# Kernel tuning notes

Measured on AMD Instinct MI355X. Metric: run time of the kernel, lower is better.

## Reference

```python
import jax, jax.numpy as jnp
import numpy as np

B, IN_DIM, H1, H2, C = 8192, 1024, 2048, 2048, 1000
E, TOP_K, RH = 8, 2, 512
QB = 127.0
EPS = 1e-5


def _ste_round(x):
    # straight-through estimator round (BitNet-style)
    return x + jax.lax.stop_gradient(jnp.round(x) - x)


def _act_quant(x):
    # per-token absmax 8-bit activation quantization
    s = QB / jnp.clip(jnp.max(jnp.abs(x), axis=-1, keepdims=True), EPS, None)
    return jnp.clip(_ste_round(x * s), -QB, QB) / s


def _weight_quant(w):
    # ternary 1.58b weight quantization, per-tensor mean-abs scale
    s = jnp.clip(jnp.mean(jnp.abs(w)), EPS, None)
    return jnp.clip(_ste_round(w / s), -1.0, 1.0) * s


def _bit_linear(x, w, b):
    return _act_quant(x) @ _weight_quant(w).T + b


def setup_inputs() -> dict:
    key = jax.random.key(0)
    ks = jax.random.split(key, 12)
    def init(k, shape, fan_in):
        return (jax.random.normal(k, shape, dtype=jnp.float32) / np.sqrt(fan_in)).astype(jnp.float32)
    return {
        "x":  jax.random.normal(ks[0], (B, IN_DIM), dtype=jnp.float32),
        "Wr1": init(ks[1], (RH, IN_DIM), IN_DIM),
        "br1": jnp.zeros((RH,), jnp.float32),
        "Wr2": init(ks[2], (E, RH), RH),
        "br2": jnp.zeros((E,), jnp.float32),
        "W1": init(ks[3], (E, H1, IN_DIM), IN_DIM),
        "b1": jnp.zeros((E, H1), jnp.float32),
        "W2": init(ks[4], (E, H2, H1), H1),
        "b2": jnp.zeros((E, H2), jnp.float32),
        "W3": init(ks[5], (E, C, H2), H2),
        "b3": jnp.zeros((E, C), jnp.float32),
    }


def _forward(x, Wr1, br1, Wr2, br2, W1, b1, W2, b2, W3, b3):
    # Router (eval mode: dropout off)
    h = jax.nn.relu(x @ Wr1.T + br1)
    router_probs = jax.nn.softmax(h @ Wr2.T + br2, axis=1)       # [B, E]
    topk_vals, topk_idx = jax.lax.top_k(router_probs, TOP_K)     # [B, K]

    # dense gate matrix: gate[b,e] = sum_k topk_vals[b,k] * (topk_idx[b,k]==e)
    gates = jnp.sum(topk_vals[..., None] * jax.nn.one_hot(topk_idx, E, dtype=x.dtype), axis=1)  # [B, E]

    def expert(w1, c1, w2, c2, w3, c3):
        y = jax.nn.relu(_bit_linear(x, w1, c1))
        y = jax.nn.relu(_bit_linear(y, w2, c2))
        return _bit_linear(y, w3, c3)                             # [B, C]

    out_all = jax.vmap(expert)(W1, b1, W2, b2, W3, b3)            # [E, B, C]
    outputs = jnp.einsum('ebc,be->bc', out_all, gates) / TOP_K    # [B, C]
    load_balancing_loss = jnp.zeros((), x.dtype)                  # eval mode
    return outputs, router_probs, load_balancing_loss


def reference(x, Wr1, br1, Wr2, br2, W1, b1, W2, b2, W3, b3):
    return _forward(x, Wr1, br1, Wr2, br2, W1, b1, W2, b2, W3, b3)
```

## Files before the change

### kernel.cpp

```cpp
#include <hip/hip_runtime.h>
#include <stdint.h>

#define DEV static __device__ __forceinline__

typedef int v4i __attribute__((ext_vector_type(4)));
typedef short v8s __attribute__((ext_vector_type(8)));
typedef float v4f __attribute__((ext_vector_type(4)));

constexpr int B_T   = 8192;
constexpr int IN_D  = 1024;
constexpr int H1D   = 2048;
constexpr int H2D   = 2048;
constexpr int CDIM  = 1000;
constexpr int NEXP  = 8;
constexpr int RHD   = 512;
constexpr float QBF  = 127.0f;
constexpr float EPSF = 1e-5f;
constexpr int NSLOT = 2 * B_T;
constexpr int MAXT  = 72;
constexpr float GAP_DELTA = 2e-3f;

DEV void load_lds16(const void* g, void* l) {
  __builtin_amdgcn_global_load_lds(
      (const __attribute__((address_space(1))) uint32_t*)(uintptr_t)g,
      (__attribute__((address_space(3))) uint32_t*)(uint32_t)(uintptr_t)l,
      16, 0, 0);
}

DEV uint32_t pack4(float a, float b, float c, float d, float s) {
  int q0 = (int)rintf(a * s); q0 = q0 > 127 ? 127 : (q0 < -127 ? -127 : q0);
  int q1 = (int)rintf(b * s); q1 = q1 > 127 ? 127 : (q1 < -127 ? -127 : q1);
  int q2 = (int)rintf(c * s); q2 = q2 > 127 ? 127 : (q2 < -127 ? -127 : q2);
  int q3 = (int)rintf(d * s); q3 = q3 > 127 ? 127 : (q3 < -127 ? -127 : q3);
  return (uint32_t)(uint8_t)q0 | ((uint32_t)(uint8_t)q1 << 8) |
         ((uint32_t)(uint8_t)q2 << 16) | ((uint32_t)(uint8_t)q3 << 24);
}

DEV uint16_t f2bf(float f) {
  uint32_t u = __float_as_uint(f);
  return (uint16_t)((u + 0x7FFFu + ((u >> 16) & 1u)) >> 16);
}
DEV float bf2f(uint16_t h) { return __uint_as_float((uint32_t)h << 16); }

__global__ __launch_bounds__(256) void wabs_reduce(const float* __restrict__ W,
                                                   long perExpert, int tbase,
                                                   double* __restrict__ partial) {
  int e = blockIdx.y;
  const float4* base = (const float4*)(W + (long)e * perExpert);
  long n4 = perExpert >> 2;
  double s = 0.0;
  for (long i = (long)blockIdx.x * 256 + threadIdx.x; i < n4; i += 32L * 256L) {
    float4 v = base[i];
    s += (double)fabsf(v.x) + (double)fabsf(v.y) + (double)fabsf(v.z) + (double)fabsf(v.w);
  }
  __shared__ double red[256];
  red[threadIdx.x] = s;
  __syncthreads();
  for (int st = 128; st > 0; st >>= 1) {
    if ((int)threadIdx.x < st) red[threadIdx.x] += red[threadIdx.x + st];
    __syncthreads();
  }
  if (threadIdx.x == 0) partial[(long)(tbase + e) * 32 + blockIdx.x] = red[0];
}

__global__ void finalize_scales(const double* __restrict__ partial, float* __restrict__ swf) {
  int t = threadIdx.x;
  if (t >= 24) return;
  double s = 0.0;
  for (int i = 0; i < 32; ++i) s += partial[t * 32 + i];
  long cnt = (t < 8) ? (long)H1D * IN_D : (t < 16) ? (long)H2D * H1D : (long)CDIM * H2D;
  float mean = (float)(s / (double)cnt);
  swf[t] = fmaxf(mean, EPSF);
}

__global__ __launch_bounds__(256) void wquant(const float* __restrict__ W,
                                              int8_t* __restrict__ Wq,
                                              const float* __restrict__ swf, int tbase,
                                              long perExpert, long total4) {
  long i = (long)blockIdx.x * 256 + threadIdx.x;
  if (i >= total4) return;
  long e = (i * 4) / perExpert;
  float s = swf[tbase + (int)e];
  float4 v = ((const float4*)W)[i];
  float t0 = fminf(fmaxf(rintf(v.x / s), -1.f), 1.f);
  float t1 = fminf(fmaxf(rintf(v.y / s), -1.f), 1.f);
  float t2 = fminf(fmaxf(rintf(v.z / s), -1.f), 1.f);
  float t3 = fminf(fmaxf(rintf(v.w / s), -1.f), 1.f);
  uint32_t p = (uint32_t)(uint8_t)(int8_t)t0 | ((uint32_t)(uint8_t)(int8_t)t1 << 8) |
               ((uint32_t)(uint8_t)(int8_t)t2 << 16) | ((uint32_t)(uint8_t)(int8_t)t3 << 24);
  ((uint32_t*)Wq)[i] = p;
}

template <int WIDTH>
__global__ __launch_bounds__(256) void actquant(const float* __restrict__ X,
                                                int8_t* __restrict__ Xq,
                                                float* __restrict__ rcp_out) {
  constexpr int PT = WIDTH / 1024;
  const int row = blockIdx.x;
  const int tid = threadIdx.x;
  const float4* src = (const float4*)(X + (size_t)row * WIDTH);
  float4 v[PT];
  float mx = 0.f;
#pragma unroll
  for (int p = 0; p < PT; ++p) {
    v[p] = src[tid * PT + p];
    mx = fmaxf(mx, fmaxf(fmaxf(fabsf(v[p].x), fabsf(v[p].y)),
                         fmaxf(fabsf(v[p].z), fabsf(v[p].w))));
  }
#pragma unroll
  for (int m = 1; m < 64; m <<= 1) mx = fmaxf(mx, __shfl_xor(mx, m));
  __shared__ float wmax[4];
  const int lane = tid & 63, w = tid >> 6;
  if (lane == 0) wmax[w] = mx;
  __syncthreads();
  mx = fmaxf(fmaxf(wmax[0], wmax[1]), fmaxf(wmax[2], wmax[3]));
  const float M = fmaxf(mx, EPSF);
  const float s = QBF / M;
  uint32_t* dst = (uint32_t*)(Xq + (size_t)row * WIDTH);
#pragma unroll
  for (int p = 0; p < PT; ++p)
    dst[tid * PT + p] = pack4(v[p].x, v[p].y, v[p].z, v[p].w, s);
  if (tid == 0) rcp_out[row] = M / QBF;
}

__global__ __launch_bounds__(256) void split_bf16(const float* __restrict__ src,
                                                  uint16_t* __restrict__ hi,
                                                  uint16_t* __restrict__ lo, long n4) {
  long i = (long)blockIdx.x * 256 + threadIdx.x;
  if (i >= n4) return;
  float4 v = ((const float4*)src)[i];
  ushort4 h, l;
  float f[4] = {v.x, v.y, v.z, v.w};
  uint16_t hh[4], ll[4];
#pragma unroll
  for (int j = 0; j < 4; ++j) {
    hh[j] = f2bf(f[j]);
    ll[j] = f2bf(f[j] - bf2f(hh[j]));
  }
  h.x = hh[0]; h.y = hh[1]; h.z = hh[2]; h.w = hh[3];
  l.x = ll[0]; l.y = ll[1]; l.z = ll[2]; l.w = ll[3];
  ((ushort4*)hi)[i] = h;
  ((ushort4*)lo)[i] = l;
}

__global__ __launch_bounds__(256, 1) void router_mfma(
    const uint16_t* __restrict__ xh, const uint16_t* __restrict__ xl,
    const uint16_t* __restrict__ wh, const uint16_t* __restrict__ wl,
    const float* __restrict__ br1, float* __restrict__ h) {
  __shared__ __align__(16) int8_t smem[2][65536];
  const int tid = threadIdx.x;
  const int lane = tid & 63, wid = tid >> 6;
  const int wm = wid >> 1, wn = wid & 1;
  const int row0 = blockIdx.x * 128, col0 = blockIdx.y * 128;

  const uint16_t* mats[4] = {xh, xl, wh, wl};
  const int rb[4] = {row0, row0, col0, col0};
  const uint8_t* src[16];
#pragma unroll
  for (int R = 0; R < 4; ++R)
#pragma unroll
    for (int i = 0; i < 4; ++i) {
      int p = i * 256 + tid;
      int r = p >> 3, c = p & 7;
      int cs = c ^ (r & 7);
      src[R * 4 + i] = (const uint8_t*)mats[R] + ((long)(rb[R] + r) * IN_D + cs * 8) * 2;
    }

  v4f acc[4][4] = {};
  auto stage = [&](int buf, int kt) {
#pragma unroll
    for (int R = 0; R < 4; ++R)
#pragma unroll
      for (int i = 0; i < 4; ++i)
        load_lds16(src[R * 4 + i] + kt * 128,
                   &smem[buf][R * 16384 + i * 4096 + wid * 1024]);
  };

  stage(0, 0);
  asm volatile("s_waitcnt vmcnt(0)" ::: "memory");
  __syncthreads();
  int buf = 0;
  for (int kt = 0; kt < 16; ++kt) {
    if (kt + 1 < 16) stage(buf ^ 1, kt + 1);
#pragma unroll
    for (int ks = 0; ks < 2; ++ks) {
      v8s ah[4], al[4], bh[4], bl[4];
#pragma unroll
      for (int m = 0; m < 4; ++m) {
        int r = wm * 64 + m * 16 + (lane & 15);
        int ch = (ks * 4 + (lane >> 4)) ^ (r & 7);
        ah[m] = *(const v8s*)&smem[buf][r * 128 + ch * 16];
        al[m] = *(const v8s*)&smem[buf][16384 + r * 128 + ch * 16];
      }
#pragma unroll
      for (int n = 0; n < 4; ++n) {
        int r = wn * 64 + n * 16 + (lane & 15);
        int ch = (ks * 4 + (lane >> 4)) ^ (r & 7);
        bh[n] = *(const v8s*)&smem[buf][32768 + r * 128 + ch * 16];
        bl[n] = *(const v8s*)&smem[buf][49152 + r * 128 + ch * 16];
      }
#pragma unroll
      for (int m = 0; m < 4; ++m)
#pragma unroll
        for (int n = 0; n < 4; ++n) {
          acc[m][n] = __builtin_amdgcn_mfma_f32_16x16x32_bf16(ah[m], bh[n], acc[m][n], 0, 0, 0);
          acc[m][n] = __builtin_amdgcn_mfma_f32_16x16x32_bf16(ah[m], bl[n], acc[m][n], 0, 0, 0);
          acc[m][n] = __builtin_amdgcn_mfma_f32_16x16x32_bf16(al[m], bh[n], acc[m][n], 0, 0, 0);
        }
    }
    asm volatile("s_waitcnt vmcnt(0)" ::: "memory");
    __syncthreads();
    buf ^= 1;
  }

  const int rbase = (lane >> 4) * 4;
  const int cfr = lane & 15;
#pragma unroll
  for (int m = 0; m < 4; ++m)
#pragma unroll
    for (int rg = 0; rg < 4; ++rg) {
      int row = row0 + wm * 64 + m * 16 + rbase + rg;
#pragma unroll
      for (int n = 0; n < 4; ++n) {
        int col = col0 + wn * 64 + n * 16 + cfr;
        h[(long)row * RHD + col] = fmaxf(acc[m][n][rg] + br1[col], 0.f);
      }
    }
}

__global__ __launch_bounds__(256) void router_stage2(const float* __restrict__ h,
                                                     const float* __restrict__ Wr2,
                                                     const float* __restrict__ br2,
                                                     float* __restrict__ probs,
                                                     int* __restrict__ idxg,
                                                     float* __restrict__ gvg,
                                                     int* __restrict__ scount,
                                                     int* __restrict__ suspects) {
  __shared__ float w2s[NEXP * RHD];
  const int tid = threadIdx.x;
  for (int i = tid; i < NEXP * RHD; i += 256) w2s[i] = Wr2[i];
  __syncthreads();
  const int lane = tid & 63, w = tid >> 6;
  const int b = blockIdx.x * 4 + w;
  const float* hrow = h + (long)b * RHD;
  float4 v0 = *(const float4*)&hrow[lane * 8];
  float4 v1 = *(const float4*)&hrow[lane * 8 + 4];
  float hr[8] = {v0.x, v0.y, v0.z, v0.w, v1.x, v1.y, v1.z, v1.w};
  float lg[8];
#pragma unroll
  for (int e = 0; e < 8; ++e) {
    float p = 0.f;
#pragma unroll
    for (int j = 0; j < 8; ++j) p = fmaf(hr[j], w2s[e * RHD + lane * 8 + j], p);
#pragma unroll
    for (int m = 1; m < 64; m <<= 1) p += __shfl_xor(p, m);
    lg[e] = p + br2[e];
  }
  if (lane == 0) {
    float mx = lg[0];
#pragma unroll
    for (int e = 1; e < 8; ++e) mx = fmaxf(mx, lg[e]);
    float ex[8], sum = 0.f;
#pragma unroll
    for (int e = 0; e < 8; ++e) { ex[e] = expf(lg[e] - mx); sum += ex[e]; }
#pragma unroll
    for (int e = 0; e < 8; ++e) probs[(long)b * 8 + e] = ex[e] / sum;
    int i0 = 0; float b0 = lg[0];
#pragma unroll
    for (int e = 1; e < 8; ++e) if (lg[e] > b0) { b0 = lg[e]; i0 = e; }
    int i1 = -1; float b1v = -3.4e38f;
#pragma unroll
    for (int e = 0; e < 8; ++e) if (e != i0 && lg[e] > b1v) { b1v = lg[e]; i1 = e; }
    float b2v = -3.4e38f;
#pragma unroll
    for (int e = 0; e < 8; ++e) if (e != i0 && e != i1 && lg[e] > b2v) b2v = lg[e];
    idxg[b * 2 + 0] = i0; idxg[b * 2 + 1] = i1;
    gvg[b * 2 + 0] = ex[i0] / sum; gvg[b * 2 + 1] = ex[i1] / sum;
    if (b1v - b2v < GAP_DELTA) {
      int p = atomicAdd(scount, 1);
      if (p < B_T) suspects[p] = b;
    }
  }
}

__global__ __launch_bounds__(256) void router_fixup(const float* __restrict__ x,
                                                    const float* __restrict__ Wr1,
                                                    const float* __restrict__ br1,
                                                    const float* __restrict__ Wr2,
                                                    const float* __restrict__ br2,
                                                    const int* __restrict__ suspects,
                                                    const int* __restrict__ scount,
                                                    float* __restrict__ probs,
                                                    int* __restrict__ idxg,
                                                    float* __restrict__ gvg) {
  __shared__ float xr[IN_D];
  __shared__ float hr[RHD];
  __shared__ float lgs[NEXP];
  const int n = *scount;
  const int tid = threadIdx.x;
  for (int s = blockIdx.x; s < n && s < B_T; s += 128) {
    const int b = suspects[s];
    __syncthreads();
    for (int i = tid; i < IN_D; i += 256) xr[i] = x[(long)b * IN_D + i];
    __syncthreads();
    {
      const int c0 = tid * 2, c1 = tid * 2 + 1;
      const float* w0 = Wr1 + (long)c0 * IN_D;
      const float* w1 = Wr1 + (long)c1 * IN_D;
      float a0 = 0.f, a1 = 0.f;
      for (int k = 0; k < IN_D; ++k) {
        float xv = xr[k];
        a0 = fmaf(xv, w0[k], a0);
        a1 = fmaf(xv, w1[k], a1);
      }
      hr[c0] = fmaxf(a0 + br1[c0], 0.f);
      hr[c1] = fmaxf(a1 + br1[c1], 0.f);
    }
    __syncthreads();
    if (tid < NEXP) {
      const float* w2 = Wr2 + (long)tid * RHD;
      float a = 0.f;
      for (int k = 0; k < RHD; ++k) a = fmaf(hr[k], w2[k], a);
      lgs[tid] = a + br2[tid];
    }
    __syncthreads();
    if (tid == 0) {
      float lg[8];
#pragma unroll
      for (int e = 0; e < 8; ++e) lg[e] = lgs[e];
      float mx = lg[0];
#pragma unroll
      for (int e = 1; e < 8; ++e) mx = fmaxf(mx, lg[e]);
      float ex[8], sum = 0.f;
#pragma unroll
      for (int e = 0; e < 8; ++e) { ex[e] = expf(lg[e] - mx); sum += ex[e]; }
#pragma unroll
      for (int e = 0; e < 8; ++e) probs[(long)b * 8 + e] = ex[e] / sum;
      int i0 = 0; float b0 = lg[0];
#pragma unroll
      for (int e = 1; e < 8; ++e) if (lg[e] > b0) { b0 = lg[e]; i0 = e; }
      int i1 = -1; float b1v = -3.4e38f;
#pragma unroll
      for (int e = 0; e < 8; ++e) if (e != i0 && lg[e] > b1v) { b1v = lg[e]; i1 = e; }
      idxg[b * 2 + 0] = i0; idxg[b * 2 + 1] = i1;
      gvg[b * 2 + 0] = ex[i0] / sum; gvg[b * 2 + 1] = ex[i1] / sum;
    }
  }
}

__global__ __launch_bounds__(256) void hist_block(const int* __restrict__ idxg,
                                                  int* __restrict__ bc) {
  __shared__ int hloc[NEXP];
  const int t = threadIdx.x;
  if (t < NEXP) hloc[t] = 0;
  __syncthreads();
  int a = blockIdx.x * 256 + t;
  atomicAdd(&hloc[idxg[a]], 1);
  __syncthreads();
  if (t < NEXP) bc[blockIdx.x * NEXP + t] = hloc[t];
}

__global__ void scan_all(const int* __restrict__ bc, int* __restrict__ blockbase,
                         int* __restrict__ ntiles, int* __restrict__ te,
                         int* __restrict__ ts, int* __restrict__ tc,
                         float* __restrict__ loss_out) {
  __shared__ int counts[NEXP], basep[NEXP];
  const int t = threadIdx.x;
  if (t < NEXP) {
    int s = 0;
    for (int b = 0; b < 64; ++b) s += bc[b * NEXP + t];
    counts[t] = s;
  }
  __syncthreads();
  if (t == 0) {
    int acc = 0, nb = 0;
    for (int e = 0; e < NEXP; ++e) {
      basep[e] = acc;
      int c = counts[e];
      int nt = (c + 255) >> 8;
      for (int i = 0; i < nt; ++i) {
        te[nb] = e; ts[nb] = acc + i * 256; tc[nb] = min(256, c - i * 256); ++nb;
      }
      acc += c;
    }
    *ntiles = nb;
    *loss_out = 0.f;
  }
  __syncthreads();
  if (t < NEXP) {
    int run = basep[t];
    for (int b = 0; b < 64; ++b) { blockbase[b * NEXP + t] = run; run += bc[b * NEXP + t]; }
  }
}

__global__ __launch_bounds__(256) void place2(const int* __restrict__ idxg,
                                              const int* __restrict__ blockbase,
                                              int* __restrict__ token_list,
                                              int* __restrict__ slotmap) {
  __shared__ int cur[NEXP];
  const int t = threadIdx.x;
  if (t < NEXP) cur[t] = blockbase[blockIdx.x * NEXP + t];
  __syncthreads();
  int a = blockIdx.x * 256 + t;
  int e = idxg[a];
  int pos = atomicAdd(&cur[e], 1);
  token_list[pos] = a >> 1;
  slotmap[a] = pos;
}

template <int KDIM, bool INDIRECT, bool RELU, bool FINAL>
__global__ __launch_bounds__(512, 1) void gemm_i8(
    const int8_t* __restrict__ Aq, const int8_t* __restrict__ Wq,
    const float* __restrict__ swf_layer, const float* __restrict__ rcp_act,
    const float* __restrict__ bias, const int* __restrict__ te,
    const int* __restrict__ ts, const int* __restrict__ tc,
    const int* __restrict__ ntiles_p, const int* __restrict__ token_list,
    float* __restrict__ Yout, int Nvalid) {
  if ((int)blockIdx.x >= *ntiles_p) return;
  extern __shared__ __align__(16) int8_t smem_dyn[];
  const int t = blockIdx.x;
  const int e = te[t], row0 = ts[t], rcount = tc[t];
  const int col0 = blockIdx.y * 256;
  const int tid = threadIdx.x;
  const int lane = tid & 63, wid = tid >> 6;
  const int wm = wid >> 2, wn = wid & 3;

  const int8_t* srcA[4];
  const int8_t* srcB[4];
#pragma unroll
  for (int i = 0; i < 4; ++i) {
    int p = i * 512 + tid;
    int r = p >> 3, c = p & 7;
    int cs = c ^ ((r >> 1) & 7);
    int ar = row0 + min(r, rcount - 1);
    long arow = INDIRECT ? (long)token_list[ar] : (long)ar;
    srcA[i] = Aq + arow * KDIM + cs * 16;
    int br = min(col0 + r, Nvalid - 1);
    srcB[i] = Wq + ((long)e * Nvalid + br) * (long)KDIM + cs * 16;
  }

  auto stage = [&](int buf, int kt) {
#pragma unroll
    for (int i = 0; i < 4; ++i) {
      int off = buf * 65536 + (i * 512 + (wid << 6)) * 16;
      load_lds16(srcA[i] + kt * 128, &smem_dyn[off]);
      load_lds16(srcB[i] + kt * 128, &smem_dyn[32768 + off]);
    }
  };

  v4i acc[8][4] = {};
  constexpr int KT = KDIM / 128;
  stage(0, 0);
  asm volatile("s_waitcnt vmcnt(0)" ::: "memory");
  __builtin_amdgcn_s_barrier();
  int buf = 0;
  for (int kt = 0; kt < KT; ++kt) {
    if (kt + 1 < KT) {
      stage(buf ^ 1, kt + 1);
      asm volatile("s_waitcnt vmcnt(8)" ::: "memory");
    } else {
      asm volatile("s_waitcnt vmcnt(0)" ::: "memory");
    }
    __builtin_amdgcn_s_barrier();
    __builtin_amdgcn_sched_barrier(0);
    const int8_t* As = &smem_dyn[buf * 65536];
    const int8_t* Bs = &smem_dyn[buf * 65536 + 32768];
#pragma unroll
    for (int ks = 0; ks < 2; ++ks) {
      v4i bv[4];
#pragma unroll
      for (int n = 0; n < 4; ++n) {
        int r = wn * 64 + n * 16 + (lane & 15);
        int cs = (ks * 4 + (lane >> 4)) ^ ((r >> 1) & 7);
        bv[n] = *(const v4i*)&Bs[r * 128 + cs * 16];
      }
#pragma unroll
      for (int m = 0; m < 8; ++m) {
        int r = wm * 128 + m * 16 + (lane & 15);
        int cs = (ks * 4 + (lane >> 4)) ^ ((r >> 1) & 7);
        v4i av = *(const v4i*)&As[r * 128 + cs * 16];
#pragma unroll
        for (int n = 0; n < 4; ++n)
          acc[m][n] = __builtin_amdgcn_mfma_i32_16x16x64_i8(av, bv[n], acc[m][n], 0, 0, 0);
      }
    }
    __builtin_amdgcn_sched_barrier(0);
    __builtin_amdgcn_s_barrier();
    buf ^= 1;
  }

  const float sw = swf_layer[e];
  const int rbase = (lane >> 4) * 4;
  const int cfr = lane & 15;
  const float* bias_e = bias + (long)e * Nvalid;
#pragma unroll
  for (int m = 0; m < 8; ++m) {
#pragma unroll
    for (int rg = 0; rg < 4; ++rg) {
      int trow = wm * 128 + m * 16 + rbase + rg;
      if (trow >= rcount) continue;
      int slot = row0 + trow;
      float rcp = rcp_act[INDIRECT ? token_list[slot] : slot];
      float dq = sw * rcp;
      if (!FINAL) {
        float* yrow = Yout + (long)slot * 2048;
#pragma unroll
        for (int n = 0; n < 4; ++n) {
          int o = col0 + wn * 64 + n * 16 + cfr;
          float v = (float)acc[m][n][rg] * dq + bias_e[o];
          if (RELU) v = fmaxf(v, 0.f);
          yrow[o] = v;
        }
      } else {
        float* zrow = Yout + (long)slot * 1024;
#pragma unroll
        for (int n = 0; n < 4; ++n) {
          int o = col0 + wn * 64 + n * 16 + cfr;
          float bb = bias_e[min(o, Nvalid - 1)];
          zrow[o] = (float)acc[m][n][rg] * dq + bb;
        }
      }
    }
  }
}

__global__ __launch_bounds__(256) void combine(const float* __restrict__ z,
                                               const int* __restrict__ slotmap,
                                               const float* __restrict__ gvg,
                                               float* __restrict__ out) {
  const int b = blockIdx.x;
  const int c = threadIdx.x;
  if (c >= 250) return;
  const int s0 = slotmap[b * 2], s1 = slotmap[b * 2 + 1];
  const float g0 = gvg[b * 2] * 0.5f, g1 = gvg[b * 2 + 1] * 0.5f;
  float4 a = *(const float4*)(z + (long)s0 * 1024 + c * 4);
  float4 q = *(const float4*)(z + (long)s1 * 1024 + c * 4);
  float4 o = {g0 * a.x + g1 * q.x, g0 * a.y + g1 * q.y,
              g0 * a.z + g1 * q.z, g0 * a.w + g1 * q.w};
  *(float4*)(out + (long)b * CDIM + c * 4) = o;
}

extern "C" void kernel_launch(void* const* d_in, const int* in_sizes, int n_in,
                              void* d_out, int out_size, void* d_ws, size_t ws_size,
                              hipStream_t stream) {
  const float* x   = (const float*)d_in[0];
  const float* Wr1 = (const float*)d_in[1];
  const float* br1 = (const float*)d_in[2];
  const float* Wr2 = (const float*)d_in[3];
  const float* br2 = (const float*)d_in[4];
  const float* W1  = (const float*)d_in[5];
  const float* b1  = (const float*)d_in[6];
  const float* W2  = (const float*)d_in[7];
  const float* b2  = (const float*)d_in[8];
  const float* W3  = (const float*)d_in[9];
  const float* b3  = (const float*)d_in[10];
  float* out = (float*)d_out;
  char* ws = (char*)d_ws;

  size_t off = 0;
  auto alloc = [&](size_t sz) { size_t r = off; off = (off + sz + 255) & ~(size_t)255; return r; };
  size_t O_META  = alloc(8192);
  size_t O_SUSP  = alloc(B_T * sizeof(int));
  size_t O_PART  = alloc(24 * 32 * sizeof(double));
  size_t O_SWF   = alloc(24 * sizeof(float));
  size_t O_RCPX  = alloc(B_T * sizeof(float));
  size_t O_IDX   = alloc(B_T * 2 * sizeof(int));
  size_t O_GVG   = alloc(B_T * 2 * sizeof(float));
  size_t O_TLIST = alloc(NSLOT * sizeof(int));
  size_t O_SLOT  = alloc(B_T * 2 * sizeof(int));
  size_t O_S1    = alloc(NSLOT * sizeof(float));
  size_t O_S2    = alloc(NSLOT * sizeof(float));
  size_t O_XQ    = alloc((size_t)B_T * IN_D);
  size_t O_WQ1   = alloc((size_t)NEXP * H1D * IN_D);
  size_t O_WQ2   = alloc((size_t)NEXP * H2D * H1D);
  size_t O_WQ3   = alloc((size_t)NEXP * CDIM * H2D);
  size_t O_YQ    = alloc((size_t)NSLOT * 2048);
  size_t O_YBIG  = alloc((size_t)NSLOT * 2048 * sizeof(float));
  (void)ws_size; (void)in_sizes; (void)n_in;

  int*    te     = (int*)(ws + O_META);
  int*    tsv    = te + 144;
  int*    tcv    = tsv + 144;
  int*    ntiles = tcv + 144;
  int*    bc     = ntiles + 4;
  int*    bbase  = bc + 512;
  int*    scount = bbase + 512;
  int*    susp   = (int*)(ws + O_SUSP);
  double* part   = (double*)(ws + O_PART);
  float*  swf    = (float*)(ws + O_SWF);
  float*  rcpx   = (float*)(ws + O_RCPX);
  int*    idxg   = (int*)(ws + O_IDX);
  float*  gvg    = (float*)(ws + O_GVG);
  int*    tlist  = (int*)(ws + O_TLIST);
  int*    slotmap= (int*)(ws + O_SLOT);
  float*  s1     = (float*)(ws + O_S1);
  float*  s2     = (float*)(ws + O_S2);
  int8_t* Xq     = (int8_t*)(ws + O_XQ);
  int8_t* wq1    = (int8_t*)(ws + O_WQ1);
  int8_t* wq2    = (int8_t*)(ws + O_WQ2);
  int8_t* wq3    = (int8_t*)(ws + O_WQ3);
  int8_t* Yq     = (int8_t*)(ws + O_YQ);
  float*  Ybig   = (float*)(ws + O_YBIG);
  float*  h      = Ybig;
  float*  zbuf   = Ybig;

  char* ybytes = (char*)Ybig;
  uint16_t* xh = (uint16_t*)(ybytes + (20l << 20));
  uint16_t* xl = (uint16_t*)(ybytes + (40l << 20));
  uint16_t* wh = (uint16_t*)(ybytes + (60l << 20));
  uint16_t* wl = (uint16_t*)(ybytes + (62l << 20));

  hipMemsetAsync(ws + O_META, 0, 8192, stream);

  wabs_reduce<<<dim3(32, 8), 256, 0, stream>>>(W1, (long)H1D * IN_D, 0, part);
  wabs_reduce<<<dim3(32, 8), 256, 0, stream>>>(W2, (long)H2D * H1D, 8, part);
  wabs_reduce<<<dim3(32, 8), 256, 0, stream>>>(W3, (long)CDIM * H2D, 16, part);
  finalize_scales<<<1, 64, 0, stream>>>(part, swf);
  wquant<<<16384, 256, 0, stream>>>(W1, wq1, swf, 0, (long)H1D * IN_D, 4194304L);
  wquant<<<32768, 256, 0, stream>>>(W2, wq2, swf, 8, (long)H2D * H1D, 8388608L);
  wquant<<<16000, 256, 0, stream>>>(W3, wq3, swf, 16, (long)CDIM * H2D, 4096000L);

  actquant<IN_D><<<B_T, 256, 0, stream>>>(x, Xq, rcpx);

  split_bf16<<<8192, 256, 0, stream>>>(x, xh, xl, (long)B_T * IN_D / 4);
  split_bf16<<<512, 256, 0, stream>>>(Wr1, wh, wl, (long)RHD * IN_D / 4);
  router_mfma<<<dim3(B_T / 128, RHD / 128), 256, 0, stream>>>(xh, xl, wh, wl, br1, h);
  router_stage2<<<B_T / 4, 256, 0, stream>>>(h, Wr2, br2, out + (size_t)B_T * CDIM,
                                             idxg, gvg, scount, susp);
  router_fixup<<<128, 256, 0, stream>>>(x, Wr1, br1, Wr2, br2, susp, scount,
                                        out + (size_t)B_T * CDIM, idxg, gvg);
  hist_block<<<64, 256, 0, stream>>>(idxg, bc);
  scan_all<<<1, 64, 0, stream>>>(bc, bbase, ntiles, te, tsv, tcv,
                                 out + (size_t)B_T * CDIM + (size_t)B_T * NEXP);
  place2<<<64, 256, 0, stream>>>(idxg, bbase, tlist, slotmap);

  gemm_i8<IN_D, true, true, false><<<dim3(MAXT, H1D / 256), 512, 131072, stream>>>(
      Xq, wq1, swf + 0, rcpx, b1, te, tsv, tcv, ntiles, tlist, Ybig, H1D);
  actquant<2048><<<NSLOT, 256, 0, stream>>>(Ybig, Yq, s1);
  gemm_i8<2048, false, true, false><<<dim3(MAXT, H2D / 256), 512, 131072, stream>>>(
      Yq, wq2, swf + 8, s1, b2, te, tsv, tcv, ntiles, tlist, Ybig, H2D);
  actquant<2048><<<NSLOT, 256, 0, stream>>>(Ybig, Yq, s2);
  gemm_i8<2048, false, false, true><<<dim3(MAXT, 1024 / 256), 512, 131072, stream>>>(
      Yq, wq3, swf + 16, s2, b3, te, tsv, tcv, ntiles, tlist, zbuf, CDIM);

  combine<<<B_T, 256, 0, stream>>>(zbuf, slotmap, gvg, out);
}
```

Measured before the change: 690.6 us.

## Restructure int8 expert GEMM into quadrant-pipelined schedule with finer prefetch

The int8 MFMA GEMM main loop is reorganized so the 256x256 tile is computed as four 128x128 quadrants per K step. Global-to-LDS prefetch is split into quarter-tile stages interleaved between quadrant MFMA phases, with s_setprio raised around the MFMA blocks and a deeper prefetch distance. The LDS swizzle changes, and launch bounds now request two blocks per CU to cut register use. The weight quantization kernel also gets a 2D grid that takes the expert index from blockIdx.y, which removes a 64-bit division per thread. The extra barriers and the lower register budget could add stalls or spills.

```diff
diff --git a/kernel.cpp b/kernel.cpp
--- a/kernel.cpp
+++ b/kernel.cpp
@@ -76,19 +76,20 @@
 __global__ __launch_bounds__(256) void wquant(const float* __restrict__ W,
                                               int8_t* __restrict__ Wq,
                                               const float* __restrict__ swf, int tbase,
-                                              long perExpert, long total4) {
+                                              long perExpert4) {
   long i = (long)blockIdx.x * 256 + threadIdx.x;
-  if (i >= total4) return;
-  long e = (i * 4) / perExpert;
-  float s = swf[tbase + (int)e];
-  float4 v = ((const float4*)W)[i];
+  if (i >= perExpert4) return;
+  int e = blockIdx.y;
+  float s = swf[tbase + e];
+  long idx = (long)e * perExpert4 + i;
+  float4 v = ((const float4*)W)[idx];
   float t0 = fminf(fmaxf(rintf(v.x / s), -1.f), 1.f);
   float t1 = fminf(fmaxf(rintf(v.y / s), -1.f), 1.f);
   float t2 = fminf(fmaxf(rintf(v.z / s), -1.f), 1.f);
   float t3 = fminf(fmaxf(rintf(v.w / s), -1.f), 1.f);
   uint32_t p = (uint32_t)(uint8_t)(int8_t)t0 | ((uint32_t)(uint8_t)(int8_t)t1 << 8) |
                ((uint32_t)(uint8_t)(int8_t)t2 << 16) | ((uint32_t)(uint8_t)(int8_t)t3 << 24);
-  ((uint32_t*)Wq)[i] = p;
+  ((uint32_t*)Wq)[idx] = p;
 }
 
 template <int WIDTH>
@@ -409,7 +410,7 @@
 }
 
 template <int KDIM, bool INDIRECT, bool RELU, bool FINAL>
-__global__ __launch_bounds__(512, 1) void gemm_i8(
+__global__ __launch_bounds__(512, 2) void gemm_i8(
     const int8_t* __restrict__ Aq, const int8_t* __restrict__ Wq,
     const float* __restrict__ swf_layer, const float* __restrict__ rcp_act,
     const float* __restrict__ bias, const int* __restrict__ te,
@@ -423,105 +424,164 @@
   const int col0 = blockIdx.y * 256;
   const int tid = threadIdx.x;
   const int lane = tid & 63, wid = tid >> 6;
-  const int wm = wid >> 2, wn = wid & 3;
-
-  const int8_t* srcA[4];
-  const int8_t* srcB[4];
-#pragma unroll
-  for (int i = 0; i < 4; ++i) {
-    int p = i * 512 + tid;
-    int r = p >> 3, c = p & 7;
-    int cs = c ^ ((r >> 1) & 7);
-    int ar = row0 + min(r, rcount - 1);
-    long arow = INDIRECT ? (long)token_list[ar] : (long)ar;
-    srcA[i] = Aq + arow * KDIM + cs * 16;
-    int br = min(col0 + r, Nvalid - 1);
-    srcB[i] = Wq + ((long)e * Nvalid + br) * (long)KDIM + cs * 16;
-  }
-
-  auto stage = [&](int buf, int kt) {
-#pragma unroll
-    for (int i = 0; i < 4; ++i) {
-      int off = buf * 65536 + (i * 512 + (wid << 6)) * 16;
-      load_lds16(srcA[i] + kt * 128, &smem_dyn[off]);
-      load_lds16(srcB[i] + kt * 128, &smem_dyn[32768 + off]);
-    }
+  const int wsm = wid >> 2, wsn = wid & 3;
+  const int fr = lane & 15, hi = lane >> 4;
+
+  const int8_t* sA[2][2];
+  const int8_t* sB[2][2];
+#pragma unroll
+  for (int hh = 0; hh < 2; ++hh)
+#pragma unroll
+    for (int i = 0; i < 2; ++i) {
+      int p = i * 512 + tid;
+      int rl = p >> 3, c = p & 7;
+      int cs = c ^ (rl & 7);
+      int rt = hh * 128 + rl;
+      int ar = row0 + min(rt, rcount - 1);
+      long arow = INDIRECT ? (long)token_list[ar] : (long)ar;
+      sA[hh][i] = Aq + arow * KDIM + cs * 16;
+      int br = min(col0 + rt, Nvalid - 1);
+      sB[hh][i] = Wq + ((long)e * Nvalid + br) * (long)KDIM + cs * 16;
+    }
+
+  auto stage = [&](int buf, int kt, int which) {
+    const int hh = which & 1;
+    const bool isB = which >= 2;
+    const int8_t* p0 = isB ? sB[hh][0] : sA[hh][0];
+    const int8_t* p1 = isB ? sB[hh][1] : sA[hh][1];
+    int base = buf * 65536 + (isB ? 32768 : 0) + hh * 16384 + wid * 1024;
+    load_lds16(p0 + (long)kt * 128, &smem_dyn[base]);
+    load_lds16(p1 + (long)kt * 128, &smem_dyn[base + 8192]);
   };
 
-  v4i acc[8][4] = {};
+  const int swz0 = ((0 * 4 + hi) ^ (fr & 7)) * 16 + fr * 128;
+  const int swz1 = ((1 * 4 + hi) ^ (fr & 7)) * 16 + fr * 128;
+
+  v4i acc[2][2][4][2] = {};
+  v4i aF[4][2];
+  v4i bF[2][2][2];
+
   constexpr int KT = KDIM / 128;
-  stage(0, 0);
-  asm volatile("s_waitcnt vmcnt(0)" ::: "memory");
-  __builtin_amdgcn_s_barrier();
-  int buf = 0;
+  stage(0, 0, 0); stage(0, 0, 1); stage(0, 0, 2); stage(0, 0, 3);
+  stage(1, 1, 0); stage(1, 1, 2); stage(1, 1, 1);
+  asm volatile("s_waitcnt vmcnt(6)" ::: "memory");
+  asm volatile("s_barrier" ::: "memory");
+
   for (int kt = 0; kt < KT; ++kt) {
-    if (kt + 1 < KT) {
-      stage(buf ^ 1, kt + 1);
-      asm volatile("s_waitcnt vmcnt(8)" ::: "memory");
+    const int buf = kt & 1;
+    const int ab = buf * 65536;
+    const int bb = ab + 32768;
+#pragma unroll
+    for (int mi = 0; mi < 4; ++mi) {
+      aF[mi][0] = *(const v4i*)&smem_dyn[ab + (wsm * 64 + mi * 16) * 128 + swz0];
+      aF[mi][1] = *(const v4i*)&smem_dyn[ab + (wsm * 64 + mi * 16) * 128 + swz1];
+    }
+#pragma unroll
+    for (int ni = 0; ni < 2; ++ni) {
+      bF[0][ni][0] = *(const v4i*)&smem_dyn[bb + (wsn * 32 + ni * 16) * 128 + swz0];
+      bF[0][ni][1] = *(const v4i*)&smem_dyn[bb + (wsn * 32 + ni * 16) * 128 + swz1];
+    }
+    if (kt + 1 < KT) stage(buf ^ 1, kt + 1, 3);
+    asm volatile("s_barrier" ::: "memory");
+    __builtin_amdgcn_s_setprio(1);
+#pragma unroll
+    for (int mi = 0; mi < 4; ++mi)
+#pragma unroll
+      for (int ni = 0; ni < 2; ++ni) {
+        acc[0][0][mi][ni] = __builtin_amdgcn_mfma_i32_16x16x64_i8(aF[mi][0], bF[0][ni][0], acc[0][0][mi][ni], 0, 0, 0);
+        acc[0][0][mi][ni] = __builtin_amdgcn_mfma_i32_16x16x64_i8(aF[mi][1], bF[0][ni][1], acc[0][0][mi][ni], 0, 0, 0);
+      }
+    __builtin_amdgcn_s_setprio(0);
+    asm volatile("s_barrier" ::: "memory");
+#pragma unroll
+    for (int ni = 0; ni < 2; ++ni) {
+      bF[1][ni][0] = *(const v4i*)&smem_dyn[bb + (128 + wsn * 32 + ni * 16) * 128 + swz0];
+      bF[1][ni][1] = *(const v4i*)&smem_dyn[bb + (128 + wsn * 32 + ni * 16) * 128 + swz1];
+    }
+    if (kt + 2 < KT) stage(buf, kt + 2, 0);
+    asm volatile("s_barrier" ::: "memory");
+    __builtin_amdgcn_s_setprio(1);
+#pragma unroll
+    for (int mi = 0; mi < 4; ++mi)
+#pragma unroll
+      for (int ni = 0; ni < 2; ++ni) {
+        acc[0][1][mi][ni] = __builtin_amdgcn_mfma_i32_16x16x64_i8(aF[mi][0], bF[1][ni][0], acc[0][1][mi][ni], 0, 0, 0);
+        acc[0][1][mi][ni] = __builtin_amdgcn_mfma_i32_16x16x64_i8(aF[mi][1], bF[1][ni][1], acc[0][1][mi][ni], 0, 0, 0);
+      }
+    __builtin_amdgcn_s_setprio(0);
+    asm volatile("s_barrier" ::: "memory");
+#pragma unroll
+    for (int mi = 0; mi < 4; ++mi) {
+      aF[mi][0] = *(const v4i*)&smem_dyn[ab + (128 + wsm * 64 + mi * 16) * 128 + swz0];
+      aF[mi][1] = *(const v4i*)&smem_dyn[ab + (128 + wsm * 64 + mi * 16) * 128 + swz1];
+    }
+    if (kt + 2 < KT) stage(buf, kt + 2, 2);
+    asm volatile("s_barrier" ::: "memory");
+    __builtin_amdgcn_s_setprio(1);
+#pragma unroll
+    for (int mi = 0; mi < 4; ++mi)
+#pragma unroll
+      for (int ni = 0; ni < 2; ++ni) {
+        acc[1][0][mi][ni] = __builtin_amdgcn_mfma_i32_16x16x64_i8(aF[mi][0], bF[0][ni][0], acc[1][0][mi][ni], 0, 0, 0);
+        acc[1][0][mi][ni] = __builtin_amdgcn_mfma_i32_16x16x64_i8(aF[mi][1], bF[0][ni][1], acc[1][0][mi][ni], 0, 0, 0);
+      }
+    __builtin_amdgcn_s_setprio(0);
+    asm volatile("s_barrier" ::: "memory");
+    if (kt + 2 < KT) stage(buf, kt + 2, 1);
+    __builtin_amdgcn_s_setprio(1);
+#pragma unroll
+    for (int mi = 0; mi < 4; ++mi)
+#pragma unroll
+      for (int ni = 0; ni < 2; ++ni) {
+        acc[1][1][mi][ni] = __builtin_amdgcn_mfma_i32_16x16x64_i8(aF[mi][0], bF[1][ni][0], acc[1][1][mi][ni], 0, 0, 0);
+        acc[1][1][mi][ni] = __builtin_amdgcn_mfma_i32_16x16x64_i8(aF[mi][1], bF[1][ni][1], acc[1][1][mi][ni], 0, 0, 0);
+      }
+    __builtin_amdgcn_s_setprio(0);
+    if (kt < KT - 3) {
+      asm volatile("s_waitcnt vmcnt(6)" ::: "memory");
     } else {
       asm volatile("s_waitcnt vmcnt(0)" ::: "memory");
     }
-    __builtin_amdgcn_s_barrier();
-    __builtin_amdgcn_sched_barrier(0);
-    const int8_t* As = &smem_dyn[buf * 65536];
-    const int8_t* Bs = &smem_dyn[buf * 65536 + 32768];
-#pragma unroll
-    for (int ks = 0; ks < 2; ++ks) {
-      v4i bv[4];
-#pragma unroll
-      for (int n = 0; n < 4; ++n) {
-        int r = wn * 64 + n * 16 + (lane & 15);
-        int cs = (ks * 4 + (lane >> 4)) ^ ((r >> 1) & 7);
-        bv[n] = *(const v4i*)&Bs[r * 128 + cs * 16];
-      }
-#pragma unroll
-      for (int m = 0; m < 8; ++m) {
-        int r = wm * 128 + m * 16 + (lane & 15);
-        int cs = (ks * 4 + (lane >> 4)) ^ ((r >> 1) & 7);
-        v4i av = *(const v4i*)&As[r * 128 + cs * 16];
-#pragma unroll
-        for (int n = 0; n < 4; ++n)
-          acc[m][n] = __builtin_amdgcn_mfma_i32_16x16x64_i8(av, bv[n], acc[m][n], 0, 0, 0);
-      }
-    }
-    __builtin_amdgcn_sched_barrier(0);
-    __builtin_amdgcn_s_barrier();
-    buf ^= 1;
+    asm volatile("s_barrier" ::: "memory");
   }
 
   const float sw = swf_layer[e];
-  const int rbase = (lane >> 4) * 4;
-  const int cfr = lane & 15;
+  const int rbase = hi * 4;
   const float* bias_e = bias + (long)e * Nvalid;
 #pragma unroll
-  for (int m = 0; m < 8; ++m) {
-#pragma unroll
-    for (int rg = 0; rg < 4; ++rg) {
-      int trow = wm * 128 + m * 16 + rbase + rg;
-      if (trow >= rcount) continue;
-      int slot = row0 + trow;
-      float rcp = rcp_act[INDIRECT ? token_list[slot] : slot];
-      float dq = sw * rcp;
-      if (!FINAL) {
-        float* yrow = Yout + (long)slot * 2048;
-#pragma unroll
-        for (int n = 0; n < 4; ++n) {
-          int o = col0 + wn * 64 + n * 16 + cfr;
-          float v = (float)acc[m][n][rg] * dq + bias_e[o];
-          if (RELU) v = fmaxf(v, 0.f);
-          yrow[o] = v;
+  for (int qm = 0; qm < 2; ++qm)
+#pragma unroll
+    for (int mi = 0; mi < 4; ++mi)
+#pragma unroll
+      for (int rg = 0; rg < 4; ++rg) {
+        int trow = qm * 128 + wsm * 64 + mi * 16 + rbase + rg;
+        if (trow >= rcount) continue;
+        int slot = row0 + trow;
+        float rcp = rcp_act[INDIRECT ? token_list[slot] : slot];
+        float dq = sw * rcp;
+        if (!FINAL) {
+          float* yrow = Yout + (long)slot * 2048;
+#pragma unroll
+          for (int qn = 0; qn < 2; ++qn)
+#pragma unroll
+            for (int ni = 0; ni < 2; ++ni) {
+              int o = col0 + qn * 128 + wsn * 32 + ni * 16 + fr;
+              float v = (float)acc[qm][qn][mi][ni][rg] * dq + bias_e[o];
+              if (RELU) v = fmaxf(v, 0.f);
+              yrow[o] = v;
+            }
+        } else {
+          float* zrow = Yout + (long)slot * 1024;
+#pragma unroll
+          for (int qn = 0; qn < 2; ++qn)
+#pragma unroll
+            for (int ni = 0; ni < 2; ++ni) {
+              int o = col0 + qn * 128 + wsn * 32 + ni * 16 + fr;
+              float bb2 = bias_e[min(o, Nvalid - 1)];
+              zrow[o] = (float)acc[qm][qn][mi][ni][rg] * dq + bb2;
+            }
         }
-      } else {
-        float* zrow = Yout + (long)slot * 1024;
-#pragma unroll
-        for (int n = 0; n < 4; ++n) {
-          int o = col0 + wn * 64 + n * 16 + cfr;
-          float bb = bias_e[min(o, Nvalid - 1)];
-          zrow[o] = (float)acc[m][n][rg] * dq + bb;
-        }
-      }
-    }
-  }
+      }
 }
 
 __global__ __launch_bounds__(256) void combine(const float* __restrict__ z,
@@ -616,9 +676,9 @@
   wabs_reduce<<<dim3(32, 8), 256, 0, stream>>>(W2, (long)H2D * H1D, 8, part);
   wabs_reduce<<<dim3(32, 8), 256, 0, stream>>>(W3, (long)CDIM * H2D, 16, part);
   finalize_scales<<<1, 64, 0, stream>>>(part, swf);
-  wquant<<<16384, 256, 0, stream>>>(W1, wq1, swf, 0, (long)H1D * IN_D, 4194304L);
-  wquant<<<32768, 256, 0, stream>>>(W2, wq2, swf, 8, (long)H2D * H1D, 8388608L);
-  wquant<<<16000, 256, 0, stream>>>(W3, wq3, swf, 16, (long)CDIM * H2D, 4096000L);
+  wquant<<<dim3(2048, 8), 256, 0, stream>>>(W1, wq1, swf, 0, 524288L);
+  wquant<<<dim3(4096, 8), 256, 0, stream>>>(W2, wq2, swf, 8, 1048576L);
+  wquant<<<dim3(2000, 8), 256, 0, stream>>>(W3, wq3, swf, 16, 512000L);
 
   actquant<IN_D><<<B_T, 256, 0, stream>>>(x, Xq, rcpx);
 
```

Measured after the change: 679.7 us. Within noise of the previous version (-1.6%).
